# Kernel tuning notes

Measured on AMD Instinct MI355X. Metric: run time of the kernel, lower is better.

Reference implementation:

```python
import jax, jax.numpy as jnp
import numpy as np

E = 1024   # embed_dim
H = 16     # num_heads
D = E // H # head_dim = 64
HD2 = D // 2
B = 2
S = 2048


def setup_inputs() -> dict:
    key = jax.random.key(0)
    ks = jax.random.split(key, 12)
    def lin(k, fan_in, fan_out):
        # xavier-uniform-ish init, stored in [in, out] (jax) convention
        lim = float(np.sqrt(6.0 / (fan_in + fan_out)))
        return jax.random.uniform(k, (fan_in, fan_out), jnp.float32, -lim, lim)
    return {
        "query": jax.random.normal(ks[0], (B, S, E), jnp.float32),
        "xi_scale": jax.random.uniform(ks[1], (B,), jnp.float32),
        "Wq": lin(ks[2], E, E), "bq": jnp.zeros((E,), jnp.float32),
        "Wk": lin(ks[3], E, E), "bk": jnp.zeros((E,), jnp.float32),
        "Wv": lin(ks[4], E, E), "bv": jnp.zeros((E,), jnp.float32),
        "Wo": lin(ks[5], E, E), "bo": jnp.zeros((E,), jnp.float32),
        "enc_w1": lin(ks[6], 1, HD2), "enc_b1": jnp.zeros((HD2,), jnp.float32),
        "ln_g": jnp.ones((HD2,), jnp.float32), "ln_b": jnp.zeros((HD2,), jnp.float32),
        "enc_w2": lin(ks[7], HD2, D), "enc_b2": jnp.zeros((D,), jnp.float32),
        "scale_gating": jnp.ones((H,), jnp.float32),
    }


def reference(query, xi_scale, Wq, bq, Wk, bk, Wv, bv, Wo, bo,
              enc_w1, enc_b1, ln_g, ln_b, enc_w2, enc_b2, scale_gating):
    b, s, e = query.shape
    h, d = H, e // H
    # --- scale adaptation: xi -> Linear -> LayerNorm -> GELU -> Linear ---
    x = xi_scale[:, None] @ enc_w1 + enc_b1                  # [B, D/2]
    mu = x.mean(-1, keepdims=True)
    var = ((x - mu) ** 2).mean(-1, keepdims=True)
    x = (x - mu) / jnp.sqrt(var + 1e-5) * ln_g + ln_b
    x = jax.nn.gelu(x, approximate=False)
    xe = x @ enc_w2 + enc_b2                                 # [B, D]
    adapt = 1.0 + jax.nn.sigmoid(scale_gating)[None, :, None] * xe[:, None, :]  # [B, H, D]
    # --- projections (self-attention: key = value = query) ---
    q = (query @ Wq + bq).reshape(b, s, h, d).transpose(0, 2, 1, 3) * adapt[:, :, None, :]
    k = (query @ Wk + bk).reshape(b, s, h, d).transpose(0, 2, 1, 3) * adapt[:, :, None, :]
    v = (query @ Wv + bv).reshape(b, s, h, d).transpose(0, 2, 1, 3)
    # --- explicit QK^T / sqrt(d) -> softmax -> V ---
    inv_scale = 1.0 / float(np.sqrt(d))
    scores = jnp.einsum('bhqd,bhkd->bhqk', q, k) * inv_scale  # [B, H, S, S]
    attn = jax.nn.softmax(scores, axis=-1)
    out = jnp.einsum('bhqk,bhkd->bhqd', attn, v)              # [B, H, S, D]
    out = out.transpose(0, 2, 1, 3).reshape(b, s, e)
    return out @ Wo + bo
```

## Files before the change

### kernel.cpp

```cpp
#include <hip/hip_runtime.h>

typedef __bf16 bf16;
typedef __attribute__((ext_vector_type(8))) __bf16 bf16x8;
typedef __attribute__((ext_vector_type(4))) float f32x4;
typedef __attribute__((ext_vector_type(16))) float f32x16;
typedef unsigned int u32;

#define MFMA16(a, b, c) __builtin_amdgcn_mfma_f32_16x16x32_bf16((a), (b), (c), 0, 0, 0)
#define MFMA32(a, b, c) __builtin_amdgcn_mfma_f32_32x32x16_bf16((a), (b), (c), 0, 0, 0)

#define BB 2
#define SS 2048
#define EE 1024
#define HH 16
#define DD 64
#define MM (BB * SS)

__device__ inline f32x4 zero4() {
    f32x4 z; z.x = 0.f; z.y = 0.f; z.z = 0.f; z.w = 0.f; return z;
}

__device__ __forceinline__ void gload16(const bf16* g, bf16* l) {
    __builtin_amdgcn_global_load_lds(
        (const __attribute__((address_space(1))) u32*)(const void*)g,
        (__attribute__((address_space(3))) u32*)(void*)l,
        16, 0, 0);
}

__device__ __forceinline__ u32 pkbf(float a, float b) {
    union { __bf16 h; unsigned short s; } ua, ub;
    ua.h = (__bf16)a; ub.h = (__bf16)b;
    return (u32)ua.s | ((u32)ub.s << 16);
}

__global__ __launch_bounds__(256) void prep_kernel(
    const float* __restrict__ query, bf16* __restrict__ qc,
    const float* __restrict__ s0, const float* __restrict__ s1,
    const float* __restrict__ s2, const float* __restrict__ s3,
    bf16* __restrict__ d0, bf16* __restrict__ d1,
    bf16* __restrict__ d2, bf16* __restrict__ d3,
    const float* __restrict__ xi, const float* __restrict__ w1,
    const float* __restrict__ b1, const float* __restrict__ lng,
    const float* __restrict__ lnb, const float* __restrict__ w2,
    const float* __restrict__ b2, const float* __restrict__ gate,
    float* __restrict__ adapt) {
    __shared__ bf16 tile[64 * 72];
    const int bid = blockIdx.x;
    const int t = threadIdx.x;

    if (bid < 2048) {
        const int i = (bid * 256 + t) * 8;
        float4 a = *(const float4*)(query + i);
        float4 b = *(const float4*)(query + i + 4);
        bf16 tmp[8];
        tmp[0] = (bf16)a.x; tmp[1] = (bf16)a.y; tmp[2] = (bf16)a.z; tmp[3] = (bf16)a.w;
        tmp[4] = (bf16)b.x; tmp[5] = (bf16)b.y; tmp[6] = (bf16)b.z; tmp[7] = (bf16)b.w;
        *(uint4*)(qc + i) = *(uint4*)tmp;
    } else if (bid < 3072) {
        const int m = (bid - 2048) >> 8;
        const int idx0 = (bid - 2048) & 255;
        const float* W = (m == 0) ? s0 : (m == 1) ? s1 : (m == 2) ? s2 : s3;
        bf16* Wt = (m == 0) ? d0 : (m == 1) ? d1 : (m == 2) ? d2 : d3;
        const int k0 = (idx0 >> 4) * 64, n0 = (idx0 & 15) * 64;
#pragma unroll
        for (int i = 0; i < 2; ++i) {
            int idx = i * 256 + t;
            int r = idx >> 3, c = (idx & 7) * 8;
            float4 a = *(const float4*)(W + (k0 + r) * EE + n0 + c);
            float4 b = *(const float4*)(W + (k0 + r) * EE + n0 + c + 4);
            bf16 tmp[8];
            tmp[0] = (bf16)a.x; tmp[1] = (bf16)a.y; tmp[2] = (bf16)a.z; tmp[3] = (bf16)a.w;
            tmp[4] = (bf16)b.x; tmp[5] = (bf16)b.y; tmp[6] = (bf16)b.z; tmp[7] = (bf16)b.w;
            *(uint4*)(tile + r * 72 + c) = *(uint4*)tmp;
        }
        __syncthreads();
#pragma unroll
        for (int i = 0; i < 2; ++i) {
            int idx = i * 256 + t;
            int n = idx >> 3, kc = (idx & 7) * 8;
            bf16 tmp[8];
#pragma unroll
            for (int j = 0; j < 8; ++j) tmp[j] = tile[(kc + j) * 72 + n];
            *(uint4*)(Wt + (n0 + n) * EE + k0 + kc) = *(uint4*)tmp;
        }
    } else {
        const int b = bid - 3072;
        float* xs = (float*)tile;
        if (t < 64) {
            const float xiv = xi[b];
            float xv = 0.f;
            if (t < 32) xv = xiv * w1[t] + b1[t];
            float sm = xv;
            for (int off = 1; off < 32; off <<= 1) sm += __shfl_xor(sm, off);
            const float mu = sm * (1.f / 32.f);
            float dv = (t < 32) ? (xv - mu) : 0.f;
            float s2 = dv * dv;
            for (int off = 1; off < 32; off <<= 1) s2 += __shfl_xor(s2, off);
            const float var = s2 * (1.f / 32.f);
            if (t < 32) {
                float xn = (xv - mu) * rsqrtf(var + 1e-5f) * lng[t] + lnb[t];
                float ge = 0.5f * xn * (1.f + erff(xn * 0.70710678118654752f));
                xs[t] = ge;
            }
        }
        __syncthreads();
        if (t < 64) {
            float acc = b2[t];
            for (int j = 0; j < 32; ++j) acc += xs[j] * w2[j * DD + t];
            for (int h = 0; h < HH; ++h) {
                float sg = 1.f / (1.f + __expf(-gate[h]));
                adapt[(b * HH + h) * DD + t] = 1.f + sg * acc;
            }
        }
    }
}

__global__ __launch_bounds__(256, 3) void gemm_qkv(
    const bf16* __restrict__ Aq, const bf16* __restrict__ Bqk,
    const bf16* __restrict__ Av,
    const float* __restrict__ bias, const float* __restrict__ bias2,
    const float* __restrict__ bias3, const float* __restrict__ adapt,
    bf16* __restrict__ outqk, bf16* __restrict__ outvt) {
    __shared__ bf16 As[2 * 128 * 32];
    __shared__ bf16 Bs[2 * 128 * 32];

    const int t = threadIdx.x;
    const int w = t >> 6, lane = t & 63;
    const int mrow = lane & 15, quad = lane >> 4;
    const int wm = (w & 1) * 64, wn = (w >> 1) * 64;

    int md, bx, by;
    const bf16 *Ap, *Bp;
    int bid = blockIdx.x;
    if (bid < 512) { md = 5; bx = bid & 31; by = bid >> 5; Ap = Aq; Bp = Bqk; }
    else { md = 4; bid -= 512; bx = bid & 7; by = bid >> 3; Ap = Av; Bp = Aq; }
    const int m0 = bx * 128, n0 = by * 128;

    f32x4 acc[4][4];
#pragma unroll
    for (int i = 0; i < 4; ++i)
#pragma unroll
        for (int j = 0; j < 4; ++j) acc[i][j] = zero4();

    const int dr = lane >> 2;
    const int dcg = ((lane & 3) ^ (dr & 3)) * 8;
    const bf16* Ag = Ap + (size_t)(m0 + w * 16 + dr) * EE + dcg;
    const bf16* Bg = Bp + (size_t)(n0 + w * 16 + dr) * EE + dcg;
    bf16* Al = As + (w * 16) * 32;
    bf16* Bl = Bs + (w * 16) * 32;

    gload16(Ag, Al);
    gload16(Ag + 64 * EE, Al + 64 * 32);
    gload16(Bg, Bl);
    gload16(Bg + 64 * EE, Bl + 64 * 32);

    for (int kt = 0; kt < 32; ++kt) {
        __syncthreads();
        if (kt < 31) {
            const int kn = (kt + 1) * 32;
            const int nb = (kt + 1) & 1;
            gload16(Ag + kn, Al + nb * 4096);
            gload16(Ag + 64 * EE + kn, Al + nb * 4096 + 64 * 32);
            gload16(Bg + kn, Bl + nb * 4096);
            gload16(Bg + 64 * EE + kn, Bl + nb * 4096 + 64 * 32);
        }
        const bf16* Ab = As + (kt & 1) * 4096;
        const bf16* Bb = Bs + (kt & 1) * 4096;
        const int sw = (quad ^ (mrow & 3)) * 8;
        bf16x8 af[4], bfr[4];
#pragma unroll
        for (int i = 0; i < 4; ++i)
            af[i] = *(const bf16x8*)(Ab + (wm + i * 16 + mrow) * 32 + sw);
#pragma unroll
        for (int j = 0; j < 4; ++j)
            bfr[j] = *(const bf16x8*)(Bb + (wn + j * 16 + mrow) * 32 + sw);
#pragma unroll
        for (int i = 0; i < 4; ++i)
#pragma unroll
            for (int j = 0; j < 4; ++j)
                acc[i][j] = MFMA16(af[i], bfr[j], acc[i][j]);
    }

#pragma unroll
    for (int i = 0; i < 4; ++i) {
#pragma unroll
        for (int j = 0; j < 4; ++j) {
            const int col = n0 + wn + j * 16 + mrow;
#pragma unroll
            for (int r = 0; r < 4; ++r) {
                const int row = m0 + wm + i * 16 + quad * 4 + r;
                float v = acc[i][j][r];
                if (md == 4) {
                    v += bias3[row];
                    const int h = row >> 6, d = row & 63;
                    const int b = col >> 11, s = col & (SS - 1);
                    outvt[(((b * HH + h) * DD + d) * SS) + s] = (bf16)v;
                } else {
                    const int m2 = col >> 10;
                    const int cl = col & 1023;
                    const int h = cl >> 6, d = cl & 63;
                    const int b = row >> 11, s = row & (SS - 1);
                    v += (m2 ? bias2[cl] : bias[cl]);
                    v *= adapt[(b * HH + h) * DD + d];
                    if (!m2) v *= 0.125f;
                    outqk[(size_t)m2 * MM * EE + ((b * HH + h) * SS + s) * DD + d] = (bf16)v;
                }
            }
        }
    }
}

__global__ __launch_bounds__(256, 3) void gemm_o(
    const bf16* __restrict__ A, const bf16* __restrict__ Bt,
    const float* __restrict__ bias, float* __restrict__ outf) {
    __shared__ bf16 As[2 * 128 * 64];
    __shared__ bf16 Bs[2 * 64 * 64];

    const int t = threadIdx.x;
    const int w = t >> 6, lane = t & 63;
    const int mrow = lane & 15, quad = lane >> 4;
    const int m0 = blockIdx.x * 128, n0 = blockIdx.y * 64;

    f32x4 acc[2][4];
#pragma unroll
    for (int i = 0; i < 2; ++i)
#pragma unroll
        for (int j = 0; j < 4; ++j) acc[i][j] = zero4();

    const int grow = lane >> 3;
    const int gsw = ((lane & 7) ^ grow) * 8;
    const bf16* Ag = A + (size_t)(m0 + w * 32 + grow) * EE + gsw;
    const bf16* Bg = Bt + (size_t)(n0 + w * 16 + grow) * EE + gsw;
    bf16* Al = As + (w * 32) * 64;
    bf16* Bl = Bs + (w * 16) * 64;

#pragma unroll
    for (int i = 0; i < 4; ++i) gload16(Ag + i * 8 * EE, Al + i * 8 * 64);
#pragma unroll
    for (int i = 0; i < 2; ++i) gload16(Bg + i * 8 * EE, Bl + i * 8 * 64);

    for (int kt = 0; kt < 16; ++kt) {
        __syncthreads();
        if (kt < 15) {
            const int kn = (kt + 1) * 64;
            const int nb = (kt + 1) & 1;
#pragma unroll
            for (int i = 0; i < 4; ++i)
                gload16(Ag + i * 8 * EE + kn, Al + nb * 8192 + i * 8 * 64);
#pragma unroll
            for (int i = 0; i < 2; ++i)
                gload16(Bg + i * 8 * EE + kn, Bl + nb * 4096 + i * 8 * 64);
        }
        const bf16* Ab = As + (kt & 1) * 8192;
        const bf16* Bb = Bs + (kt & 1) * 4096;
#pragma unroll
        for (int ks = 0; ks < 2; ++ks) {
            const int cg = ks * 4 + quad;
            const int sw = (cg ^ (mrow & 7)) * 8;
            bf16x8 af[2], bfr[4];
#pragma unroll
            for (int mi = 0; mi < 2; ++mi)
                af[mi] = *(const bf16x8*)(Ab + (w * 32 + mi * 16 + mrow) * 64 + sw);
#pragma unroll
            for (int nj = 0; nj < 4; ++nj)
                bfr[nj] = *(const bf16x8*)(Bb + (nj * 16 + mrow) * 64 + sw);
#pragma unroll
            for (int mi = 0; mi < 2; ++mi)
#pragma unroll
                for (int nj = 0; nj < 4; ++nj)
                    acc[mi][nj] = MFMA16(af[mi], bfr[nj], acc[mi][nj]);
        }
    }

#pragma unroll
    for (int mi = 0; mi < 2; ++mi) {
#pragma unroll
        for (int nj = 0; nj < 4; ++nj) {
            const int col = n0 + nj * 16 + mrow;
#pragma unroll
            for (int r = 0; r < 4; ++r) {
                const int row = m0 + w * 32 + mi * 16 + quad * 4 + r;
                outf[row * EE + col] = acc[mi][nj][r] + bias[col];
            }
        }
    }
}

__global__ __launch_bounds__(256, 2) void attn_kernel(
    const bf16* __restrict__ q, const bf16* __restrict__ k,
    const bf16* __restrict__ vt, bf16* __restrict__ o0, bf16* __restrict__ o1,
    float* __restrict__ lws) {
    __shared__ bf16 lds[16896];
    bf16* Ks = lds;
    bf16* Vs = lds + 8192;

    const int t = threadIdx.x;
    const int w = t >> 6, lane = t & 63;
    const int q32 = lane & 31, h = lane >> 5;
    const int split = blockIdx.x >> 8;
    const int rest = blockIdx.x & 255;
    const int bh = rest >> 3;
    const int qb = rest & 7;
    const int qr0 = qb * 256 + w * 64;

    bf16x8 qf[2][4];
#pragma unroll
    for (int qi = 0; qi < 2; ++qi)
#pragma unroll
        for (int c = 0; c < 4; ++c)
            qf[qi][c] = *(const bf16x8*)(q + (size_t)(bh * SS + qr0 + qi * 32 + q32) * DD +
                                         c * 16 + h * 8);

    f32x16 oacc[2][2];
#pragma unroll
    for (int qi = 0; qi < 2; ++qi)
#pragma unroll
        for (int mf = 0; mf < 2; ++mf)
#pragma unroll
            for (int i = 0; i < 16; ++i) oacc[qi][mf][i] = 0.f;
    float lsum[2] = {0.f, 0.f};

    const int dr = lane >> 3;
    const int dcg = ((lane & 7) ^ dr) * 8;
    const bf16* kg = k + (size_t)bh * SS * DD;
    const bf16* vg = vt + (size_t)bh * DD * SS;
    const bf16* kgl = kg + (size_t)dr * DD + dcg;
    const bf16* vgl = vg + (size_t)(w * 16 + dr) * SS + dcg;

    const int ktbeg = split * (SS / 128), ktend = ktbeg + (SS / 128);

#pragma unroll
    for (int i = 0; i < 2; ++i) {
        const int rb = w * 16 + i * 8;
        gload16(kgl + (size_t)(ktbeg * 64 + rb) * DD, Ks + rb * 64);
        gload16(vgl + (size_t)(i * 8) * SS + ktbeg * 64, Vs + rb * 64);
    }

    for (int kt = ktbeg; kt < ktend; ++kt) {
        __syncthreads();
        if (kt < ktend - 1) {
            const int nb = (kt + 1) & 1;
#pragma unroll
            for (int i = 0; i < 2; ++i) {
                const int rb = w * 16 + i * 8;
                gload16(kgl + (size_t)((kt + 1) * 64 + rb) * DD, Ks + nb * 4096 + rb * 64);
                gload16(vgl + (size_t)(i * 8) * SS + (kt + 1) * 64, Vs + nb * 4096 + rb * 64);
            }
        }
        const bf16* Kb = Ks + (kt & 1) * 4096;
        const bf16* Vb = Vs + (kt & 1) * 4096;

        f32x16 st[2][2];
#pragma unroll
        for (int qi = 0; qi < 2; ++qi)
#pragma unroll
            for (int mf = 0; mf < 2; ++mf)
#pragma unroll
                for (int i = 0; i < 16; ++i) st[qi][mf][i] = 0.f;
#pragma unroll
        for (int c = 0; c < 4; ++c) {
            const int sw = ((2 * c + h) ^ (q32 & 7)) * 8;
#pragma unroll
            for (int mf = 0; mf < 2; ++mf) {
                bf16x8 kf = *(const bf16x8*)(Kb + (mf * 32 + q32) * 64 + sw);
#pragma unroll
                for (int qi = 0; qi < 2; ++qi)
                    st[qi][mf] = MFMA32(kf, qf[qi][c], st[qi][mf]);
            }
        }

        u32 P32[2][2][8];
#pragma unroll
        for (int qi = 0; qi < 2; ++qi)
#pragma unroll
            for (int mf = 0; mf < 2; ++mf)
#pragma unroll
                for (int rp = 0; rp < 8; ++rp) {
                    float pa = __expf(st[qi][mf][2 * rp]);
                    float pb = __expf(st[qi][mf][2 * rp + 1]);
                    lsum[qi] += pa + pb;
                    P32[qi][mf][rp] = pkbf(pa, pb);
                }

#pragma unroll
        for (int c = 0; c < 4; ++c) {
            const int mfs = c >> 1;
            const int ro = (c & 1) * 4;
            union { u32 u[4]; bf16x8 v; } pb[2];
#pragma unroll
            for (int qi = 0; qi < 2; ++qi) {
                u32 vA0 = P32[qi][mfs][ro + 0], vA1 = P32[qi][mfs][ro + 1];
                u32 vB0 = P32[qi][mfs][ro + 2], vB1 = P32[qi][mfs][ro + 3];
                u32 prep0 = h ? vA0 : vB0;
                u32 prep1 = h ? vA1 : vB1;
                u32 sh0 = __shfl_xor(prep0, 32);
                u32 sh1 = __shfl_xor(prep1, 32);
                pb[qi].u[0] = h ? sh0 : vA0;
                pb[qi].u[1] = h ? sh1 : vA1;
                pb[qi].u[2] = h ? vB0 : sh0;
                pb[qi].u[3] = h ? vB1 : sh1;
            }
            const int sw = ((2 * c + h) ^ (q32 & 7)) * 8;
#pragma unroll
            for (int mf = 0; mf < 2; ++mf) {
                bf16x8 vf = *(const bf16x8*)(Vb + (mf * 32 + q32) * 64 + sw);
#pragma unroll
                for (int qi = 0; qi < 2; ++qi)
                    oacc[qi][mf] = MFMA32(vf, pb[qi].v, oacc[qi][mf]);
            }
        }
    }

    lsum[0] += __shfl_xor(lsum[0], 32);
    lsum[1] += __shfl_xor(lsum[1], 32);

    __syncthreads();
    bf16* ob = lds + w * 4224;
#pragma unroll
    for (int qi = 0; qi < 2; ++qi)
#pragma unroll
        for (int mf = 0; mf < 2; ++mf)
#pragma unroll
            for (int rp = 0; rp < 8; ++rp) {
                const int d = 32 * mf + 2 * (rp & 1) + 8 * (rp >> 1) + 4 * h;
                *(u32*)(ob + (qi * 32 + q32) * 66 + d) =
                    pkbf(oacc[qi][mf][2 * rp], oacc[qi][mf][2 * rp + 1]);
            }
    __builtin_amdgcn_s_waitcnt(0);

    bf16* op = split ? o1 : o0;
    const int b = bh >> 4, head = bh & 15;
    const int half = lane & 1;
#pragma unroll
    for (int p = 0; p < 2; ++p) {
        const int r = p * 32 + (lane >> 1);
#pragma unroll
        for (int i = 0; i < 4; ++i) {
            bf16x8 val = *(const bf16x8*)(ob + r * 66 + half * 32 + i * 8);
            *(bf16x8*)(op + (size_t)(b * SS + qr0 + r) * EE + head * DD +
                       half * 32 + i * 8) = val;
        }
    }
    if (lane < 32) {
#pragma unroll
        for (int qi = 0; qi < 2; ++qi)
            lws[split * (32 * SS) + bh * SS + qr0 + qi * 32 + q32] = lsum[qi];
    }
}

__global__ __launch_bounds__(256) void combine_kernel(
    const bf16* __restrict__ p1, const float* __restrict__ lws,
    bf16* __restrict__ o) {
    const int i = (blockIdx.x * 256 + threadIdx.x) * 8;
    const int b = i >> 21, s = (i >> 10) & (SS - 1), h = (i >> 6) & 15;
    const int li = (b * HH + h) * SS + s;
    const float inv = 1.f / (lws[li] + lws[32 * SS + li]);
    uint4 u0 = *(const uint4*)(o + i);
    uint4 u1 = *(const uint4*)(p1 + i);
    bf16 a0[8], a1[8], res[8];
    *(uint4*)a0 = u0; *(uint4*)a1 = u1;
#pragma unroll
    for (int j = 0; j < 8; ++j) res[j] = (bf16)(((float)a0[j] + (float)a1[j]) * inv);
    *(uint4*)(o + i) = *(uint4*)res;
}

extern "C" void kernel_launch(void* const* d_in, const int* in_sizes, int n_in,
                              void* d_out, int out_size, void* d_ws, size_t ws_size,
                              hipStream_t stream) {
    const float* query = (const float*)d_in[0];
    const float* xi    = (const float*)d_in[1];
    const float* Wq = (const float*)d_in[2];  const float* bq = (const float*)d_in[3];
    const float* Wk = (const float*)d_in[4];  const float* bk = (const float*)d_in[5];
    const float* Wv = (const float*)d_in[6];  const float* bv = (const float*)d_in[7];
    const float* Wo = (const float*)d_in[8];  const float* bo = (const float*)d_in[9];
    const float* ew1 = (const float*)d_in[10]; const float* eb1 = (const float*)d_in[11];
    const float* lng = (const float*)d_in[12]; const float* lnb = (const float*)d_in[13];
    const float* ew2 = (const float*)d_in[14]; const float* eb2 = (const float*)d_in[15];
    const float* gate = (const float*)d_in[16];
    float* out = (float*)d_out;

    char* ws = (char*)d_ws;
    const size_t SZ = (size_t)MM * EE * sizeof(bf16);
    bf16* queryc = (bf16*)(ws);
    bf16* p0     = (bf16*)(ws);
    bf16* qws    = (bf16*)(ws + SZ);
    bf16* kws    = (bf16*)(ws + 2 * SZ);
    bf16* wqT    = (bf16*)(ws + 3 * SZ);
    bf16* wkT    = (bf16*)(ws + 3 * SZ + 2097152);
    bf16* wvT    = (bf16*)(ws + 3 * SZ + 2 * 2097152);
    bf16* woT    = (bf16*)(ws + 3 * SZ + 3 * 2097152);
    float* adaptws = (float*)(ws + 4 * SZ);
    float* lws   = (float*)(ws + 4 * SZ + 8192);
    bf16* vtws   = (bf16*)d_out;
    bf16* p1     = (bf16*)((char*)d_out + SZ);

    prep_kernel<<<3074, 256, 0, stream>>>(query, queryc, Wq, Wk, Wv, Wo,
                                          wqT, wkT, wvT, woT,
                                          xi, ew1, eb1, lng, lnb, ew2, eb2, gate,
                                          adaptws);

    gemm_qkv<<<768, 256, 0, stream>>>(queryc, wqT, wvT, bq, bk, bv, adaptws,
                                      qws, vtws);

    attn_kernel<<<2 * BB * HH * (SS / 256), 256, 0, stream>>>(qws, kws, vtws, p0, p1, lws);
    combine_kernel<<<MM * EE / (256 * 8), 256, 0, stream>>>(p1, lws, p0);

    gemm_o<<<dim3(MM / 128, EE / 64), 256, 0, stream>>>(p0, woT, bo, out);
}
```

Before: 224.2 us.

## Shrink attention blocks to two waves with 32-key tiles and fold log2e into exp2

The attention kernel now runs 128-thread blocks (two waves, 128 query rows) over 32-key K/V tiles instead of 256-thread blocks with 64-key tiles. That doubles the grid and halves LDS per block, which should allow more resident blocks per CU. The V^T tile gets a new LDS layout and swizzle. Separately, the Q scale now folds in log2(e) so the softmax can use the hardware exp2 directly instead of __expf. The trade-off is twice as many loop iterations and barriers per key range, and less K/V reuse per LDS load.

```diff
diff --git a/kernel.cpp b/kernel.cpp
--- a/kernel.cpp
+++ b/kernel.cpp
@@ -202,7 +202,7 @@
                     const int b = row >> 11, s = row & (SS - 1);
                     v += (m2 ? bias2[cl] : bias[cl]);
                     v *= adapt[(b * HH + h) * DD + d];
-                    if (!m2) v *= 0.125f;
+                    if (!m2) v *= 0.18033688011113811f;
                     outqk[(size_t)m2 * MM * EE + ((b * HH + h) * SS + s) * DD + d] = (bf16)v;
                 }
             }
@@ -286,22 +286,22 @@
     }
 }
 
-__global__ __launch_bounds__(256, 2) void attn_kernel(
+__global__ __launch_bounds__(128, 4) void attn_kernel(
     const bf16* __restrict__ q, const bf16* __restrict__ k,
     const bf16* __restrict__ vt, bf16* __restrict__ o0, bf16* __restrict__ o1,
     float* __restrict__ lws) {
-    __shared__ bf16 lds[16896];
+    __shared__ bf16 lds[8448];
     bf16* Ks = lds;
-    bf16* Vs = lds + 8192;
+    bf16* Vs = lds + 4096;
 
     const int t = threadIdx.x;
     const int w = t >> 6, lane = t & 63;
     const int q32 = lane & 31, h = lane >> 5;
-    const int split = blockIdx.x >> 8;
-    const int rest = blockIdx.x & 255;
-    const int bh = rest >> 3;
-    const int qb = rest & 7;
-    const int qr0 = qb * 256 + w * 64;
+    const int split = blockIdx.x >> 9;
+    const int rest = blockIdx.x & 511;
+    const int bh = rest >> 4;
+    const int qb = rest & 15;
+    const int qr0 = qb * 128 + w * 64;
 
     bf16x8 qf[2][4];
 #pragma unroll
@@ -320,20 +320,22 @@
             for (int i = 0; i < 16; ++i) oacc[qi][mf][i] = 0.f;
     float lsum[2] = {0.f, 0.f};
 
-    const int dr = lane >> 3;
-    const int dcg = ((lane & 7) ^ dr) * 8;
+    const int kdr = lane >> 3;
+    const int kdc = ((lane & 7) ^ kdr) * 8;
+    const int vdr = lane >> 2;
+    const int vdc = ((lane & 3) ^ (vdr & 3)) * 8;
+
     const bf16* kg = k + (size_t)bh * SS * DD;
     const bf16* vg = vt + (size_t)bh * DD * SS;
-    const bf16* kgl = kg + (size_t)dr * DD + dcg;
-    const bf16* vgl = vg + (size_t)(w * 16 + dr) * SS + dcg;
-
-    const int ktbeg = split * (SS / 128), ktend = ktbeg + (SS / 128);
+    const bf16* kgl = kg + (size_t)(w * 16 + kdr) * DD + kdc;
+    const bf16* vgl = vg + (size_t)(w * 32 + vdr) * SS + vdc;
+
+    const int ktbeg = split * (SS / 64), ktend = ktbeg + (SS / 64);
 
 #pragma unroll
     for (int i = 0; i < 2; ++i) {
-        const int rb = w * 16 + i * 8;
-        gload16(kgl + (size_t)(ktbeg * 64 + rb) * DD, Ks + rb * 64);
-        gload16(vgl + (size_t)(i * 8) * SS + ktbeg * 64, Vs + rb * 64);
+        gload16(kgl + (size_t)(ktbeg * 32 + i * 8) * DD, Ks + (w * 16 + i * 8) * 64);
+        gload16(vgl + (size_t)(i * 16) * SS + ktbeg * 32, Vs + (w * 32 + i * 16) * 32);
     }
 
     for (int kt = ktbeg; kt < ktend; ++kt) {
@@ -342,55 +344,48 @@
             const int nb = (kt + 1) & 1;
 #pragma unroll
             for (int i = 0; i < 2; ++i) {
-                const int rb = w * 16 + i * 8;
-                gload16(kgl + (size_t)((kt + 1) * 64 + rb) * DD, Ks + nb * 4096 + rb * 64);
-                gload16(vgl + (size_t)(i * 8) * SS + (kt + 1) * 64, Vs + nb * 4096 + rb * 64);
-            }
-        }
-        const bf16* Kb = Ks + (kt & 1) * 4096;
-        const bf16* Vb = Vs + (kt & 1) * 4096;
-
-        f32x16 st[2][2];
+                gload16(kgl + (size_t)((kt + 1) * 32 + i * 8) * DD,
+                        Ks + nb * 2048 + (w * 16 + i * 8) * 64);
+                gload16(vgl + (size_t)(i * 16) * SS + (kt + 1) * 32,
+                        Vs + nb * 2048 + (w * 32 + i * 16) * 32);
+            }
+        }
+        const bf16* Kb = Ks + (kt & 1) * 2048;
+        const bf16* Vb = Vs + (kt & 1) * 2048;
+
+        f32x16 st[2];
 #pragma unroll
         for (int qi = 0; qi < 2; ++qi)
 #pragma unroll
-            for (int mf = 0; mf < 2; ++mf)
-#pragma unroll
-                for (int i = 0; i < 16; ++i) st[qi][mf][i] = 0.f;
+            for (int i = 0; i < 16; ++i) st[qi][i] = 0.f;
 #pragma unroll
         for (int c = 0; c < 4; ++c) {
             const int sw = ((2 * c + h) ^ (q32 & 7)) * 8;
-#pragma unroll
-            for (int mf = 0; mf < 2; ++mf) {
-                bf16x8 kf = *(const bf16x8*)(Kb + (mf * 32 + q32) * 64 + sw);
-#pragma unroll
-                for (int qi = 0; qi < 2; ++qi)
-                    st[qi][mf] = MFMA32(kf, qf[qi][c], st[qi][mf]);
-            }
-        }
-
-        u32 P32[2][2][8];
+            bf16x8 kf = *(const bf16x8*)(Kb + q32 * 64 + sw);
+#pragma unroll
+            for (int qi = 0; qi < 2; ++qi)
+                st[qi] = MFMA32(kf, qf[qi][c], st[qi]);
+        }
+
+        u32 P32[2][8];
 #pragma unroll
         for (int qi = 0; qi < 2; ++qi)
 #pragma unroll
-            for (int mf = 0; mf < 2; ++mf)
-#pragma unroll
-                for (int rp = 0; rp < 8; ++rp) {
-                    float pa = __expf(st[qi][mf][2 * rp]);
-                    float pb = __expf(st[qi][mf][2 * rp + 1]);
-                    lsum[qi] += pa + pb;
-                    P32[qi][mf][rp] = pkbf(pa, pb);
-                }
-
-#pragma unroll
-        for (int c = 0; c < 4; ++c) {
-            const int mfs = c >> 1;
-            const int ro = (c & 1) * 4;
+            for (int rp = 0; rp < 8; ++rp) {
+                float pa = __builtin_amdgcn_exp2f(st[qi][2 * rp]);
+                float pb = __builtin_amdgcn_exp2f(st[qi][2 * rp + 1]);
+                lsum[qi] += pa + pb;
+                P32[qi][rp] = pkbf(pa, pb);
+            }
+
+#pragma unroll
+        for (int c = 0; c < 2; ++c) {
+            const int ro = c * 4;
             union { u32 u[4]; bf16x8 v; } pb[2];
 #pragma unroll
             for (int qi = 0; qi < 2; ++qi) {
-                u32 vA0 = P32[qi][mfs][ro + 0], vA1 = P32[qi][mfs][ro + 1];
-                u32 vB0 = P32[qi][mfs][ro + 2], vB1 = P32[qi][mfs][ro + 3];
+                u32 vA0 = P32[qi][ro + 0], vA1 = P32[qi][ro + 1];
+                u32 vB0 = P32[qi][ro + 2], vB1 = P32[qi][ro + 3];
                 u32 prep0 = h ? vA0 : vB0;
                 u32 prep1 = h ? vA1 : vB1;
                 u32 sh0 = __shfl_xor(prep0, 32);
@@ -400,10 +395,11 @@
                 pb[qi].u[2] = h ? vB0 : sh0;
                 pb[qi].u[3] = h ? vB1 : sh1;
             }
-            const int sw = ((2 * c + h) ^ (q32 & 7)) * 8;
 #pragma unroll
             for (int mf = 0; mf < 2; ++mf) {
-                bf16x8 vf = *(const bf16x8*)(Vb + (mf * 32 + q32) * 64 + sw);
+                const int vrow = mf * 32 + q32;
+                const int sw = ((2 * c + h) ^ (vrow & 3)) * 8;
+                bf16x8 vf = *(const bf16x8*)(Vb + vrow * 32 + sw);
 #pragma unroll
                 for (int qi = 0; qi < 2; ++qi)
                     oacc[qi][mf] = MFMA32(vf, pb[qi].v, oacc[qi][mf]);
@@ -502,7 +498,7 @@
     gemm_qkv<<<768, 256, 0, stream>>>(queryc, wqT, wvT, bq, bk, bv, adaptws,
                                       qws, vtws);
 
-    attn_kernel<<<2 * BB * HH * (SS / 256), 256, 0, stream>>>(qws, kws, vtws, p0, p1, lws);
+    attn_kernel<<<1024, 128, 0, stream>>>(qws, kws, vtws, p0, p1, lws);
     combine_kernel<<<MM * EE / (256 * 8), 256, 0, stream>>>(p1, lws, p0);
 
     gemm_o<<<dim3(MM / 128, EE / 64), 256, 0, stream>>>(p0, woT, bo, out);
```

Measured after the change: 295.0 us. +31.6%, slower.
